# Kernel optimization log

Hardware: AMD Instinct MI355X
Metric: run time of the kernel (lower is better)

## Reference

```python
import jax, jax.numpy as jnp
import numpy as np

NUM_CLASSES = 19
C_ENET = 1.02            # ENet weighting constant
THRESH = -float(np.log(0.7))  # -log(thresh)
N_MIN = 262144           # hard-example floor (B*H*W // 16)


def setup_inputs() -> dict:
    key = jax.random.key(0)
    k1, k2 = jax.random.split(key)
    logits = jax.random.normal(k1, (8, NUM_CLASSES, 512, 1024), dtype=jnp.float32)
    labels = jax.random.randint(k2, (8, 512, 1024), 0, NUM_CLASSES, dtype=jnp.int32)
    return {"logits": logits, "labels": labels}


def reference(logits, labels):
    # ENet class weights from label histogram: w_c = 1 / ln(c + freq_c)
    flat_lab = labels.reshape(-1)
    total = flat_lab.shape[0]
    counts = jnp.bincount(flat_lab, length=NUM_CLASSES).astype(jnp.float32)
    propensity = counts / jnp.float32(total)
    class_weights = 1.0 / jnp.log(C_ENET + propensity)  # [C]

    # weighted per-pixel cross entropy (reduction='none')
    logp = jax.nn.log_softmax(logits, axis=1)                       # [B,C,H,W]
    nll = -jnp.take_along_axis(logp, labels[:, None].astype(jnp.int32), axis=1)[:, 0]  # [B,H,W]
    loss = (class_weights[labels] * nll).reshape(-1)                # [B*H*W]

    # OHEM: sort descending, keep > thresh if n_min-th loss exceeds thresh, else top n_min
    loss_sorted = jnp.sort(loss)[::-1]
    cond = loss_sorted[N_MIN] > THRESH
    idx = jnp.arange(loss_sorted.shape[0])
    mask = jnp.where(cond, loss_sorted > THRESH, idx < N_MIN).astype(loss_sorted.dtype)
    return jnp.sum(loss_sorted * mask) / jnp.sum(mask)
```

## Files before the change

### kernel.cpp

```cpp
#include <hip/hip_runtime.h>
#include <math.h>

#define NCLS   19
#define HW     (512*1024)
#define BHW    (8*HW)
#define NQ     (BHW/4)
#define GRID_H (NQ/256)
#define GRID_L (BHW/256)
#define NSLOT  64
#define KSEL   262144u
#define THRESH 0.35667494393873245f

struct Meta {
  double Spart[NSLOT];
  unsigned int Kpart[NSLOT];
  unsigned int done0;
  unsigned int _pad[3];
  unsigned int counts[32];
  float weights[32];
};

__global__ __launch_bounds__(256) void k_hist_weights(const int* __restrict__ lab,
                                                      Meta* __restrict__ m) {
  __shared__ unsigned int h[32];
  if (threadIdx.x < 32) h[threadIdx.x] = 0u;
  __syncthreads();
  int q = blockIdx.x * 256 + threadIdx.x;
  int4 l = reinterpret_cast<const int4*>(lab)[q];
  atomicAdd(&h[l.x], 1u);
  atomicAdd(&h[l.y], 1u);
  atomicAdd(&h[l.z], 1u);
  atomicAdd(&h[l.w], 1u);
  __syncthreads();
  if (threadIdx.x < 32) {
    unsigned int c = h[threadIdx.x];
    if (c) atomicAdd(&m->counts[threadIdx.x], c);
  }
  __syncthreads();
  if (threadIdx.x == 0) {
    __threadfence();
    unsigned int done = atomicAdd(&m->done0, 1u);
    if (done == GRID_H - 1u) {
      for (int c = 0; c < NCLS; ++c) {
        unsigned int cnt = atomicAdd(&m->counts[c], 0u);
        float p = (float)cnt * (1.0f / (float)BHW);
        m->weights[c] = 1.0f / logf(1.02f + p);
      }
    }
  }
}

__global__ __launch_bounds__(256) void k_loss(const float* __restrict__ logits,
                                              const int* __restrict__ lab,
                                              float* __restrict__ loss,
                                              Meta* __restrict__ m) {
  __shared__ float w[NCLS];
  __shared__ float sp[4];
  __shared__ unsigned int cp[4];
  if (threadIdx.x < NCLS) w[threadIdx.x] = m->weights[threadIdx.x];
  __syncthreads();

  int p  = blockIdx.x * 256 + threadIdx.x;
  int b  = p >> 19;
  int hw = p & (HW - 1);
  const float* lp = logits + (size_t)b * (NCLS * HW) + hw;
  int lbl = lab[p];

  float v[NCLS];
#pragma unroll
  for (int c = 0; c < NCLS; ++c) v[c] = lp[c * HW];

  float mx = v[0];
#pragma unroll
  for (int c = 1; c < NCLS; ++c) mx = fmaxf(mx, v[c]);

  float s = 0.f, x = 0.f;
#pragma unroll
  for (int c = 0; c < NCLS; ++c) {
    s += __expf(v[c] - mx);
    x = (c == lbl) ? v[c] : x;
  }
  float o = w[lbl] * (mx + logf(s) - x);
  loss[p] = o;

  float ls = (o > THRESH) ? o : 0.f;
  unsigned int lc = (o > THRESH) ? 1u : 0u;
#pragma unroll
  for (int off = 32; off > 0; off >>= 1) {
    ls += __shfl_down(ls, off);
    lc += __shfl_down(lc, off);
  }
  int wid = threadIdx.x >> 6;
  if ((threadIdx.x & 63) == 0) { sp[wid] = ls; cp[wid] = lc; }
  __syncthreads();
  if (threadIdx.x == 0) {
    float bs = sp[0] + sp[1] + sp[2] + sp[3];
    unsigned int bc = cp[0] + cp[1] + cp[2] + cp[3];
    int slot = blockIdx.x & (NSLOT - 1);
    atomicAdd(&m->Spart[slot], (double)bs);
    atomicAdd(&m->Kpart[slot], bc);
  }
}

__global__ __launch_bounds__(1024) void k_final(const float* __restrict__ loss,
                                                Meta* __restrict__ m,
                                                float* __restrict__ out) {
  __shared__ unsigned int h[2048];
  __shared__ unsigned int sel[4];
  __shared__ double dsp[16];
  __shared__ unsigned int dcp[16];

  const int T = 1024;
  int tid = threadIdx.x;

  __shared__ double Stot_s; __shared__ unsigned int Ktot_s;
  if (tid == 0) {
    double S = 0.0; unsigned int K = 0u;
    for (int i = 0; i < NSLOT; ++i) { S += m->Spart[i]; K += m->Kpart[i]; }
    Stot_s = S; Ktot_s = K;
    if (K > KSEL) out[0] = (float)(S / (double)K);
  }
  __syncthreads();
  unsigned int K = Ktot_s;
  if (K > KSEL) return;

  for (int i = tid; i < 2048; i += T) h[i] = 0u;
  __syncthreads();
  for (int q = tid; q < NQ; q += T) {
    float4 v = reinterpret_cast<const float4*>(loss)[q];
    atomicAdd(&h[__float_as_uint(v.x) >> 21], 1u);
    atomicAdd(&h[__float_as_uint(v.y) >> 21], 1u);
    atomicAdd(&h[__float_as_uint(v.z) >> 21], 1u);
    atomicAdd(&h[__float_as_uint(v.w) >> 21], 1u);
  }
  __syncthreads();
  if (tid == 0) {
    unsigned int cum = 0;
    for (int b = 2047; b >= 0; --b) {
      unsigned int hb = h[b];
      if (cum + hb >= KSEL) { sel[0] = (unsigned)b; sel[3] = KSEL - cum; break; }
      cum += hb;
    }
  }
  __syncthreads();
  unsigned int b1 = sel[0], k1 = sel[3];

  for (int i = tid; i < 2048; i += T) h[i] = 0u;
  __syncthreads();
  for (int q = tid; q < NQ; q += T) {
    float4 v = reinterpret_cast<const float4*>(loss)[q];
    unsigned int bx = __float_as_uint(v.x), by = __float_as_uint(v.y);
    unsigned int bz = __float_as_uint(v.z), bw = __float_as_uint(v.w);
    if ((bx >> 21) == b1) atomicAdd(&h[(bx >> 10) & 2047u], 1u);
    if ((by >> 21) == b1) atomicAdd(&h[(by >> 10) & 2047u], 1u);
    if ((bz >> 21) == b1) atomicAdd(&h[(bz >> 10) & 2047u], 1u);
    if ((bw >> 21) == b1) atomicAdd(&h[(bw >> 10) & 2047u], 1u);
  }
  __syncthreads();
  if (tid == 0) {
    unsigned int cum = 0;
    for (int b = 2047; b >= 0; --b) {
      unsigned int hb = h[b];
      if (cum + hb >= k1) { sel[1] = (unsigned)b; sel[3] = k1 - cum; break; }
      cum += hb;
    }
  }
  __syncthreads();
  unsigned int b2 = sel[1], k2 = sel[3];
  unsigned int pre = (b1 << 11) | b2;

  for (int i = tid; i < 1024; i += T) h[i] = 0u;
  __syncthreads();
  for (int q = tid; q < NQ; q += T) {
    float4 v = reinterpret_cast<const float4*>(loss)[q];
    unsigned int bx = __float_as_uint(v.x), by = __float_as_uint(v.y);
    unsigned int bz = __float_as_uint(v.z), bw = __float_as_uint(v.w);
    if ((bx >> 10) == pre) atomicAdd(&h[bx & 1023u], 1u);
    if ((by >> 10) == pre) atomicAdd(&h[by & 1023u], 1u);
    if ((bz >> 10) == pre) atomicAdd(&h[bz & 1023u], 1u);
    if ((bw >> 10) == pre) atomicAdd(&h[bw & 1023u], 1u);
  }
  __syncthreads();
  if (tid == 0) {
    unsigned int cum = 0;
    for (int b = 1023; b >= 0; --b) {
      unsigned int hb = h[b];
      if (cum + hb >= k2) { sel[2] = (b1 << 21) | (b2 << 10) | (unsigned)b; break; }
      cum += hb;
    }
  }
  __syncthreads();
  unsigned int vb = sel[2];

  double ls = 0.0; unsigned int lc = 0u;
  for (int q = tid; q < NQ; q += T) {
    float4 v = reinterpret_cast<const float4*>(loss)[q];
    if (__float_as_uint(v.x) > vb) { ls += (double)v.x; ++lc; }
    if (__float_as_uint(v.y) > vb) { ls += (double)v.y; ++lc; }
    if (__float_as_uint(v.z) > vb) { ls += (double)v.z; ++lc; }
    if (__float_as_uint(v.w) > vb) { ls += (double)v.w; ++lc; }
  }
#pragma unroll
  for (int off = 32; off > 0; off >>= 1) {
    ls += __shfl_down(ls, off);
    lc += __shfl_down(lc, off);
  }
  int wid = tid >> 6;
  if ((tid & 63) == 0) { dsp[wid] = ls; dcp[wid] = lc; }
  __syncthreads();
  if (tid == 0) {
    double sumV = 0.0; unsigned int cntV = 0u;
    for (int i = 0; i < 16; ++i) { sumV += dsp[i]; cntV += dcp[i]; }
    float v = __uint_as_float(vb);
    double top = sumV + (double)(KSEL - cntV) * (double)v;
    out[0] = (float)(top / (double)KSEL);
  }
}

extern "C" void kernel_launch(void* const* d_in, const int* in_sizes, int n_in,
                              void* d_out, int out_size, void* d_ws, size_t ws_size,
                              hipStream_t stream) {
  const float* logits = (const float*)d_in[0];
  const int*   labels = (const int*)d_in[1];
  float* out  = (float*)d_out;
  float* loss = (float*)d_ws;
  Meta*  meta = (Meta*)((char*)d_ws + (size_t)BHW * 4);

  hipMemsetAsync(meta, 0, sizeof(Meta), stream);
  k_hist_weights<<<GRID_H, 256, 0, stream>>>(labels, meta);
  k_loss        <<<GRID_L, 256, 0, stream>>>(logits, labels, loss, meta);
  k_final       <<<1, 1024, 0, stream>>>(loss, meta, out);
}
```

Baseline: 213.4 us.

## Vectorize loss kernel to four pixels per thread with online softmax

```diff
diff --git a/kernel.cpp b/kernel.cpp
--- a/kernel.cpp
+++ b/kernel.cpp
@@ -5,8 +5,7 @@
 #define HW     (512*1024)
 #define BHW    (8*HW)
 #define NQ     (BHW/4)
-#define GRID_H (NQ/256)
-#define GRID_L (BHW/256)
+#define GRID_Q (NQ/256)
 #define NSLOT  64
 #define KSEL   262144u
 #define THRESH 0.35667494393873245f
@@ -20,6 +19,12 @@
   float weights[32];
 };
 
+__global__ __launch_bounds__(256) void k_init(Meta* __restrict__ m) {
+  unsigned int* p = (unsigned int*)m;
+  const int n = (int)(sizeof(Meta) / 4);
+  for (int i = threadIdx.x; i < n; i += 256) p[i] = 0u;
+}
+
 __global__ __launch_bounds__(256) void k_hist_weights(const int* __restrict__ lab,
                                                       Meta* __restrict__ m) {
   __shared__ unsigned int h[32];
@@ -40,7 +45,7 @@
   if (threadIdx.x == 0) {
     __threadfence();
     unsigned int done = atomicAdd(&m->done0, 1u);
-    if (done == GRID_H - 1u) {
+    if (done == GRID_Q - 1u) {
       for (int c = 0; c < NCLS; ++c) {
         unsigned int cnt = atomicAdd(&m->counts[c], 0u);
         float p = (float)cnt * (1.0f / (float)BHW);
@@ -50,41 +55,58 @@
   }
 }
 
-__global__ __launch_bounds__(256) void k_loss(const float* __restrict__ logits,
-                                              const int* __restrict__ lab,
-                                              float* __restrict__ loss,
-                                              Meta* __restrict__ m) {
+__global__ __launch_bounds__(256, 8) void k_loss(const float* __restrict__ logits,
+                                                 const int* __restrict__ lab,
+                                                 float* __restrict__ loss,
+                                                 Meta* __restrict__ m) {
   __shared__ float w[NCLS];
   __shared__ float sp[4];
   __shared__ unsigned int cp[4];
   if (threadIdx.x < NCLS) w[threadIdx.x] = m->weights[threadIdx.x];
   __syncthreads();
 
-  int p  = blockIdx.x * 256 + threadIdx.x;
-  int b  = p >> 19;
-  int hw = p & (HW - 1);
+  int q = blockIdx.x * 256 + threadIdx.x;
+  int base = q << 2;
+  int b  = base >> 19;
+  int hw = base & (HW - 1);
   const float* lp = logits + (size_t)b * (NCLS * HW) + hw;
-  int lbl = lab[p];
-
-  float v[NCLS];
+  int4 l4 = reinterpret_cast<const int4*>(lab)[q];
+
+  float4 v = *reinterpret_cast<const float4*>(lp);
+  float m0 = v.x, m1 = v.y, m2 = v.z, m3 = v.w;
+  float s0 = 1.f, s1 = 1.f, s2 = 1.f, s3 = 1.f;
+  float x0 = (l4.x == 0) ? v.x : 0.f;
+  float x1 = (l4.y == 0) ? v.y : 0.f;
+  float x2 = (l4.z == 0) ? v.z : 0.f;
+  float x3 = (l4.w == 0) ? v.w : 0.f;
+
 #pragma unroll
-  for (int c = 0; c < NCLS; ++c) v[c] = lp[c * HW];
-
-  float mx = v[0];
-#pragma unroll
-  for (int c = 1; c < NCLS; ++c) mx = fmaxf(mx, v[c]);
-
-  float s = 0.f, x = 0.f;
-#pragma unroll
-  for (int c = 0; c < NCLS; ++c) {
-    s += __expf(v[c] - mx);
-    x = (c == lbl) ? v[c] : x;
-  }
-  float o = w[lbl] * (mx + logf(s) - x);
-  loss[p] = o;
-
-  float ls = (o > THRESH) ? o : 0.f;
-  unsigned int lc = (o > THRESH) ? 1u : 0u;
+  for (int c = 1; c < NCLS; ++c) {
+    lp += HW;
+    float4 t = *reinterpret_cast<const float4*>(lp);
+    float nm;
+    nm = fmaxf(m0, t.x); s0 = s0 * __expf(m0 - nm) + __expf(t.x - nm); m0 = nm;
+    nm = fmaxf(m1, t.y); s1 = s1 * __expf(m1 - nm) + __expf(t.y - nm); m1 = nm;
+    nm = fmaxf(m2, t.z); s2 = s2 * __expf(m2 - nm) + __expf(t.z - nm); m2 = nm;
+    nm = fmaxf(m3, t.w); s3 = s3 * __expf(m3 - nm) + __expf(t.w - nm); m3 = nm;
+    x0 = (c == l4.x) ? t.x : x0;
+    x1 = (c == l4.y) ? t.y : x1;
+    x2 = (c == l4.z) ? t.z : x2;
+    x3 = (c == l4.w) ? t.w : x3;
+  }
+
+  float4 o;
+  o.x = w[l4.x] * (m0 + logf(s0) - x0);
+  o.y = w[l4.y] * (m1 + logf(s1) - x1);
+  o.z = w[l4.z] * (m2 + logf(s2) - x2);
+  o.w = w[l4.w] * (m3 + logf(s3) - x3);
+  reinterpret_cast<float4*>(loss)[q] = o;
+
+  float ls = 0.f; unsigned int lc = 0u;
+  if (o.x > THRESH) { ls += o.x; ++lc; }
+  if (o.y > THRESH) { ls += o.y; ++lc; }
+  if (o.z > THRESH) { ls += o.z; ++lc; }
+  if (o.w > THRESH) { ls += o.w; ++lc; }
 #pragma unroll
   for (int off = 32; off > 0; off >>= 1) {
     ls += __shfl_down(ls, off);
@@ -113,11 +135,11 @@
   const int T = 1024;
   int tid = threadIdx.x;
 
-  __shared__ double Stot_s; __shared__ unsigned int Ktot_s;
+  __shared__ unsigned int Ktot_s;
   if (tid == 0) {
     double S = 0.0; unsigned int K = 0u;
     for (int i = 0; i < NSLOT; ++i) { S += m->Spart[i]; K += m->Kpart[i]; }
-    Stot_s = S; Ktot_s = K;
+    Ktot_s = K;
     if (K > KSEL) out[0] = (float)(S / (double)K);
   }
   __syncthreads();
@@ -226,8 +248,8 @@
   float* loss = (float*)d_ws;
   Meta*  meta = (Meta*)((char*)d_ws + (size_t)BHW * 4);
 
-  hipMemsetAsync(meta, 0, sizeof(Meta), stream);
-  k_hist_weights<<<GRID_H, 256, 0, stream>>>(labels, meta);
-  k_loss        <<<GRID_L, 256, 0, stream>>>(logits, labels, loss, meta);
+  k_init        <<<1, 256, 0, stream>>>(meta);
+  k_hist_weights<<<GRID_Q, 256, 0, stream>>>(labels, meta);
+  k_loss        <<<GRID_Q, 256, 0, stream>>>(logits, labels, loss, meta);
   k_final       <<<1, 1024, 0, stream>>>(loss, meta, out);
 }
```

New measurement: 201.1 us. -5.8%, faster.
